# Kernel tuning notes

Measured on AMD Instinct MI355X. Metric: run time of the kernel, lower is better.

## Reference

```python
import jax, jax.numpy as jnp
import numpy as np

N = 65536       # active voxels
C = 128         # embed_channels
DEPTH = 4
NSEG = 1024     # number of clusters per level
K = 27          # 3x3x3 kernel taps
LRELU = 0.01
EPS_BN = 1e-5


def _bn(x, g, b):
    # training-mode batchnorm over the voxel axis (biased variance, as torch)
    m = jnp.mean(x, axis=0)
    v = jnp.var(x, axis=0)
    return (x - m) * jax.lax.rsqrt(v + EPS_BN) * g + b


def _lrelu(x):
    return jnp.where(x >= 0, x, LRELU * x)


def _proj(x, w, g, b):
    # Linear(bias=False) -> BatchNorm1d -> LeakyReLU
    return _lrelu(_bn(x @ w, g, b))


def setup_inputs() -> dict:
    key = jax.random.key(0)
    ks = jax.random.split(key, 24)
    s = 1.0 / np.sqrt(C)
    sc = 1.0 / np.sqrt(K * C)
    u = lambda k, shp, sk: jax.random.uniform(k, shp, jnp.float32, -sk, sk)
    g = lambda k, shp: 1.0 + 0.1 * jax.random.normal(k, shp, jnp.float32)
    inp = {}
    inp['feat'] = jax.random.normal(ks[0], (N, C), jnp.float32)
    inp['clusters'] = jax.random.randint(ks[1], (DEPTH - 1, N), 0, NSEG)
    # neighbor table for 3x3x3 sparse conv; value == N means neighbor absent
    inp['neighbor_idx'] = jax.random.randint(ks[2], (N, K), 0, N + 1)
    inp['lw_w'] = u(ks[3], (DEPTH - 1, C, C), s)
    inp['lw_gamma'] = g(ks[4], (DEPTH - 1, C))
    inp['lw_beta'] = 0.1 * jax.random.normal(ks[5], (DEPTH - 1, C), jnp.float32)
    inp['w_w'] = u(ks[6], (DEPTH - 1, C, C), s)
    inp['proj_w'] = u(ks[7], (DEPTH, C, C), s)
    inp['proj_gamma'] = g(ks[8], (DEPTH, C))
    inp['proj_beta'] = 0.1 * jax.random.normal(ks[9], (DEPTH, C), jnp.float32)
    inp['adaptive_w'] = u(ks[10], (C, DEPTH - 1), s)
    inp['fuse_w'] = u(ks[11], (2 * C, C), 1.0 / np.sqrt(2 * C))
    inp['fuse_gamma'] = g(ks[12], (C,))
    inp['fuse_beta'] = 0.1 * jax.random.normal(ks[13], (C,), jnp.float32)
    inp['conv1_w'] = u(ks[14], (K, C, C), sc)
    inp['conv2_w'] = u(ks[15], (K, C, C), sc)
    inp['bn1_gamma'] = g(ks[16], (C,))
    inp['bn1_beta'] = 0.1 * jax.random.normal(ks[17], (C,), jnp.float32)
    inp['bn2_gamma'] = g(ks[18], (C,))
    inp['bn2_beta'] = 0.1 * jax.random.normal(ks[19], (C,), jnp.float32)
    return inp


def _forward(feat, clusters, neighbor_idx, lw_w, lw_gamma, lw_beta, w_w,
             proj_w, proj_gamma, proj_beta, adaptive_w, fuse_w, fuse_gamma,
             fuse_beta, conv1_w, conv2_w, bn1_gamma, bn1_beta, bn2_gamma,
             bn2_beta):
    x_in = feat
    feats = []
    for i in range(DEPTH - 1):
        c = clusters[i]
        pw = _proj(feat, lw_w[i], lw_gamma[i], lw_beta[i])          # [N,C]
        cnt = jnp.maximum(
            jax.ops.segment_sum(jnp.ones((N,), feat.dtype), c, num_segments=NSEG), 1.0)
        seg_mean = jax.ops.segment_sum(pw, c, num_segments=NSEG) / cnt[:, None]
        pw = pw - seg_mean[c]                                        # center per cluster
        pw = pw @ w_w[i]
        pw = jnp.exp(pw - jnp.max(pw))                               # global max, as in source
        pw = pw / (jax.ops.segment_sum(pw, c, num_segments=NSEG)[c] + 1e-6)
        pf = _proj(feat, proj_w[i], proj_gamma[i], proj_beta[i]) * pw
        feats.append(jax.ops.segment_sum(pf, c, num_segments=NSEG)[c])
    adp = jax.nn.softmax(feat @ adaptive_w, axis=1)                  # [N,3]
    feats = jnp.stack(feats, axis=1)                                 # [N,3,C]
    agg = jnp.einsum('ld,ldc->lc', adp, feats)                       # [N,C]
    f_last = _proj(feat, proj_w[DEPTH - 1], proj_gamma[DEPTH - 1], proj_beta[DEPTH - 1])
    fused = _proj(jnp.concatenate([f_last, agg], axis=1), fuse_w, fuse_gamma, fuse_beta) + x_in
    residual = fused
    # 3x3x3 sparse conv on fixed topology: 27 masked gathers + per-tap GEMM
    mask = (neighbor_idx < N).astype(fused.dtype)                    # [N,K]
    idx = jnp.minimum(neighbor_idx, N - 1)

    def sconv(x, w):
        out = jnp.zeros((N, C), x.dtype)
        for k in range(K):
            out = out + (jnp.take(x, idx[:, k], axis=0) * mask[:, k:k + 1]) @ w[k]
        return out

    d = _lrelu(_bn(sconv(fused, conv1_w), bn1_gamma, bn1_beta))
    d = _lrelu(_bn(sconv(d, conv2_w), bn2_gamma, bn2_beta) + residual)
    return d


def reference(feat, clusters, neighbor_idx, lw_w, lw_gamma, lw_beta, w_w,
              proj_w, proj_gamma, proj_beta, adaptive_w, fuse_w, fuse_gamma,
              fuse_beta, conv1_w, conv2_w, bn1_gamma, bn1_beta, bn2_gamma,
              bn2_beta):
    return _forward(feat, clusters, neighbor_idx, lw_w, lw_gamma, lw_beta,
                    w_w, proj_w, proj_gamma, proj_beta, adaptive_w, fuse_w,
                    fuse_gamma, fuse_beta, conv1_w, conv2_w, bn1_gamma,
                    bn1_beta, bn2_gamma, bn2_beta)
```

## Files before the change

kernel.cpp:

```cpp
#include <hip/hip_runtime.h>

typedef unsigned short u16;
typedef unsigned int u32;
typedef __attribute__((ext_vector_type(8))) short bf16x8;
typedef __attribute__((ext_vector_type(4))) float f32x4;
typedef __attribute__((ext_vector_type(4))) u32 u32x4;

#define NROWS 65536
#define CCH 128
#define PE ((size_t)65537*128)

__device__ __forceinline__ float bf2f(u16 x){ u32 u=((u32)x)<<16; return __builtin_bit_cast(float,u); }
__device__ __forceinline__ u16 f2bf(float f){ u32 u=__builtin_bit_cast(u32,f); u += 0x7fffu + ((u>>16)&1u); return (u16)(u>>16); }
__device__ __forceinline__ float lrelu(float v){ return v>=0.f? v : 0.01f*v; }
__device__ __forceinline__ u32 fenc(float f){ u32 u=__builtin_bit_cast(u32,f); return (u & 0x80000000u) ? ~u : (u | 0x80000000u); }
__device__ __forceinline__ float fdec(u32 u){ u32 b = (u & 0x80000000u) ? (u ^ 0x80000000u) : ~u; return __builtin_bit_cast(float,b); }

__global__ __launch_bounds__(256) void prep_transpose(
    const float* __restrict__ lw, const float* __restrict__ ww, const float* __restrict__ pj,
    const float* __restrict__ fw, const float* __restrict__ c1, const float* __restrict__ c2,
    u16* __restrict__ WT)
{
  int i = blockIdx.x*256 + threadIdx.x;
  float v;
  if (i < 49152)      { int j=i;        int m=j>>14,e=j&16383,n=e>>7,k=e&127; v=lw[(m<<14)+(k<<7)+n]; }
  else if (i < 98304) { int j=i-49152;  int m=j>>14,e=j&16383,n=e>>7,k=e&127; v=ww[(m<<14)+(k<<7)+n]; }
  else if (i < 163840){ int j=i-98304;  int m=j>>14,e=j&16383,n=e>>7,k=e&127; v=pj[(m<<14)+(k<<7)+n]; }
  else if (i < 196608){ int j=i-163840; int n=j>>8, k=j&255;                  v=fw[(k<<7)+n]; }
  else if (i < 638976){ int j=i-196608; int m=j>>14,e=j&16383,n=e>>7,k=e&127; v=c1[(m<<14)+(k<<7)+n]; }
  else                { int j=i-638976; int m=j>>14,e=j&16383,n=e>>7,k=e&127; v=c2[(m<<14)+(k<<7)+n]; }
  WT[i]=f2bf(v);
}

__global__ __launch_bounds__(256) void nbrT_k(const int* __restrict__ nbr, int* __restrict__ nbrT){
  __shared__ int s[64*27];
  int b = blockIdx.x;
  for (int i=threadIdx.x; i<64*27; i+=256) s[i] = nbr[b*64*27 + i];
  __syncthreads();
  for (int i=threadIdx.x; i<64*27; i+=256){
    int tap=i>>6, row=i&63;
    nbrT[(size_t)tap*NROWS + b*64 + row] = s[row*27 + tap];
  }
}

__global__ __launch_bounds__(256) void hist_k(const int* __restrict__ cl, int* __restrict__ cnt){
  int i = blockIdx.x*256 + threadIdx.x;
  int l = i>>16;
  atomicAdd(&cnt[l*1024 + cl[i]], 1);
}
__global__ __launch_bounds__(1024) void scan_k(const int* __restrict__ cnt, int* __restrict__ starts, int* __restrict__ cur){
  int l = blockIdx.x, t = threadIdx.x;
  __shared__ int s[1024];
  int v = cnt[l*1024+t];
  s[t]=v; __syncthreads();
  for (int off=1; off<1024; off<<=1){
    int u_ = (t>=off) ? s[t-off] : 0;
    __syncthreads();
    s[t] += u_;
    __syncthreads();
  }
  int incl=s[t], excl=incl-v;
  starts[l*1025+t]=excl;
  if (t==1023) starts[l*1025+1024]=incl;
  cur[l*1024+t]=excl;
}
__global__ __launch_bounds__(256) void scatter_k(const int* __restrict__ cl, int* __restrict__ cur, int* __restrict__ order){
  int i = blockIdx.x*256 + threadIdx.x;
  int l = i>>16;
  int c = cl[i];
  int p = atomicAdd(&cur[l*1024+c], 1);
  order[l*65536 + p] = i & 65535;
}

struct BS7 { const u16* BT[7]; u16* out[7]; float* stats[7]; };

__global__ __launch_bounds__(256,2) void gemm_feat7(const float* __restrict__ feat, BS7 p)
{
  const int tid=threadIdx.x, lane=tid&63, quad=lane>>4, l15=lane&15;
  const int w=tid>>6, rh=w>>1, chq=w&1;
  const int row0=blockIdx.x*128;

  __shared__ __align__(16) u16 ldsA[128*136];
  __shared__ float cs[256];

  #pragma unroll
  for (int it=0; it<8; ++it){
    int row = it*16 + (tid>>4), chn = tid&15;
    const float* Af = feat + (size_t)(row0+row)*CCH + chn*8;
    float4 lo = *(const float4*)(Af);
    float4 hi = *(const float4*)(Af+4);
    u32x4 d;
    d[0]=(u32)f2bf(lo.x)|((u32)f2bf(lo.y)<<16);
    d[1]=(u32)f2bf(lo.z)|((u32)f2bf(lo.w)<<16);
    d[2]=(u32)f2bf(hi.x)|((u32)f2bf(hi.y)<<16);
    d[3]=(u32)f2bf(hi.z)|((u32)f2bf(hi.w)<<16);
    *(u32x4*)(&ldsA[row*136 + chn*8]) = d;
  }
  __syncthreads();

  #pragma unroll 1
  for (int y=0; y<7; ++y){
    const u16* Bb = p.BT[y];
    f32x4 acc[4][4];
    #pragma unroll
    for (int a_=0;a_<4;++a_)
      #pragma unroll
      for (int b_=0;b_<4;++b_) acc[a_][b_]=(f32x4){0.f,0.f,0.f,0.f};
    #pragma unroll
    for (int ks=0; ks<4; ++ks){
      bf16x8 af[4], bfv[4];
      #pragma unroll
      for (int mb=0;mb<4;++mb)
        af[mb]=*(const bf16x8*)(&ldsA[(rh*64+mb*16+l15)*136 + ks*32 + quad*8]);
      #pragma unroll
      for (int nb=0;nb<4;++nb)
        bfv[nb]=*(const bf16x8*)(Bb + (size_t)(chq*64+nb*16+l15)*CCH + ks*32 + quad*8);
      #pragma unroll
      for (int mb=0;mb<4;++mb)
        #pragma unroll
        for (int nb=0;nb<4;++nb)
          acc[mb][nb]=__builtin_amdgcn_mfma_f32_16x16x32_bf16(af[mb],bfv[nb],acc[mb][nb],0,0,0);
    }
    u16* O = p.out[y];
    #pragma unroll
    for (int mb=0;mb<4;++mb){
      int rbase=row0+rh*64+mb*16+quad*4;
      #pragma unroll
      for (int e=0;e<4;++e)
        #pragma unroll
        for (int nb=0;nb<4;++nb)
          O[(size_t)(rbase+e)*CCH + chq*64+nb*16+l15]=f2bf(acc[mb][nb][e]);
    }
    __syncthreads();
    cs[tid]=0.f;
    __syncthreads();
    #pragma unroll
    for (int nb=0;nb<4;++nb){
      float s=0.f,s2=0.f;
      #pragma unroll
      for (int mb=0;mb<4;++mb)
        #pragma unroll
        for (int e=0;e<4;++e){ float v=acc[mb][nb][e]; s+=v; s2+=v*v; }
      s += __shfl_xor(s,16);  s += __shfl_xor(s,32);
      s2+= __shfl_xor(s2,16); s2+= __shfl_xor(s2,32);
      if (lane<16){
        int col=chq*64+nb*16+l15;
        atomicAdd(&cs[col],s); atomicAdd(&cs[128+col],s2);
      }
    }
    __syncthreads();
    atomicAdd(&p.stats[y][tid], cs[tid]);
  }
}

struct BS3 { const u16* A[3]; const u16* BT[3]; float* out[3]; u32* gmax[3]; };

__global__ __launch_bounds__(256,2) void gemm_w3(BS3 p)
{
  const int tid=threadIdx.x, lane=tid&63, quad=lane>>4, l15=lane&15;
  const int w=tid>>6, rh=w>>1, chq=w&1;
  const int row0=blockIdx.x*128;
  const int y=blockIdx.y;

  __shared__ __align__(16) u16 ldsA[128*136];
  __shared__ float wred[4];

  const u16* A = p.A[y];
  #pragma unroll
  for (int it=0; it<8; ++it){
    int row = it*16 + (tid>>4), chn = tid&15;
    *(u32x4*)(&ldsA[row*136 + chn*8]) = *(const u32x4*)(A + (size_t)(row0+row)*CCH + chn*8);
  }
  __syncthreads();

  const u16* Bb = p.BT[y];
  f32x4 acc[4][4];
  #pragma unroll
  for (int a_=0;a_<4;++a_)
    #pragma unroll
    for (int b_=0;b_<4;++b_) acc[a_][b_]=(f32x4){0.f,0.f,0.f,0.f};
  #pragma unroll
  for (int ks=0; ks<4; ++ks){
    bf16x8 af[4], bfv[4];
    #pragma unroll
    for (int mb=0;mb<4;++mb)
      af[mb]=*(const bf16x8*)(&ldsA[(rh*64+mb*16+l15)*136 + ks*32 + quad*8]);
    #pragma unroll
    for (int nb=0;nb<4;++nb)
      bfv[nb]=*(const bf16x8*)(Bb + (size_t)(chq*64+nb*16+l15)*CCH + ks*32 + quad*8);
    #pragma unroll
    for (int mb=0;mb<4;++mb)
      #pragma unroll
      for (int nb=0;nb<4;++nb)
        acc[mb][nb]=__builtin_amdgcn_mfma_f32_16x16x32_bf16(af[mb],bfv[nb],acc[mb][nb],0,0,0);
  }
  float* O = p.out[y];
  float m=-3.0e38f;
  #pragma unroll
  for (int mb=0;mb<4;++mb){
    int rbase=row0+rh*64+mb*16+quad*4;
    #pragma unroll
    for (int e=0;e<4;++e)
      #pragma unroll
      for (int nb=0;nb<4;++nb){
        float v=acc[mb][nb][e];
        O[(size_t)(rbase+e)*CCH + chq*64+nb*16+l15]=v;
        m=fmaxf(m,v);
      }
  }
  #pragma unroll
  for (int o=1;o<64;o<<=1) m=fmaxf(m,__shfl_xor(m,o));
  if (lane==0) wred[w]=m;
  __syncthreads();
  if (tid==0){
    float mm=fmaxf(fmaxf(wred[0],wred[1]),fmaxf(wred[2],wred[3]));
    atomicMax(p.gmax[y], fenc(mm));
  }
}

__global__ __launch_bounds__(256,2) void gemm_fuse(
    const u16* __restrict__ A0, const u16* __restrict__ A1,
    const float* __restrict__ tstat, const float* __restrict__ tg, const float* __restrict__ tb,
    const u16* __restrict__ BT, u16* __restrict__ out, float* __restrict__ stats)
{
  const int tid=threadIdx.x, lane=tid&63, quad=lane>>4, l15=lane&15;
  const int w=tid>>6, rh=w>>1, chq=w&1;
  const int row0=blockIdx.x*128;

  __shared__ __align__(16) u16 ldsA[128*136];
  __shared__ float tsc[128], tsh[128];
  __shared__ float cs[256];

  if (tid<128){
    float s=tstat[tid], s2=tstat[128+tid];
    float mean=s*(1.0f/65536.0f);
    float var =s2*(1.0f/65536.0f)-mean*mean;
    float rstd=rsqrtf(var+1e-5f);
    float scv =tg[tid]*rstd;
    tsc[tid]=scv; tsh[tid]=tb[tid]-mean*scv;
  }

  f32x4 acc[4][4];
  #pragma unroll
  for (int a_=0;a_<4;++a_)
    #pragma unroll
    for (int b_=0;b_<4;++b_) acc[a_][b_]=(f32x4){0.f,0.f,0.f,0.f};

  #pragma unroll 1
  for (int tap=0; tap<2; ++tap){
    __syncthreads();
    const u16* Ab = tap ? A1 : A0;
    #pragma unroll
    for (int it=0; it<8; ++it){
      int row = it*16 + (tid>>4), chn = tid&15;
      u32x4 d = *(const u32x4*)(Ab + (size_t)(row0+row)*CCH + chn*8);
      if (tap==0){
        #pragma unroll
        for (int pq=0;pq<4;++pq){
          u32 xv=d[pq]; int k=chn*8+2*pq;
          float f0=lrelu(tsc[k  ]*bf2f((u16)(xv&0xffffu))+tsh[k  ]);
          float f1=lrelu(tsc[k+1]*bf2f((u16)(xv>>16))    +tsh[k+1]);
          d[pq]=(u32)f2bf(f0)|((u32)f2bf(f1)<<16);
        }
      }
      *(u32x4*)(&ldsA[row*136 + chn*8]) = d;
    }
    __syncthreads();
    const u16* Bb = BT + tap*128;
    #pragma unroll
    for (int ks=0; ks<4; ++ks){
      bf16x8 af[4], bfv[4];
      #pragma unroll
      for (int mb=0;mb<4;++mb)
        af[mb]=*(const bf16x8*)(&ldsA[(rh*64+mb*16+l15)*136 + ks*32 + quad*8]);
      #pragma unroll
      for (int nb=0;nb<4;++nb)
        bfv[nb]=*(const bf16x8*)(Bb + (size_t)(chq*64+nb*16+l15)*256 + ks*32 + quad*8);
      #pragma unroll
      for (int mb=0;mb<4;++mb)
        #pragma unroll
        for (int nb=0;nb<4;++nb)
          acc[mb][nb]=__builtin_amdgcn_mfma_f32_16x16x32_bf16(af[mb],bfv[nb],acc[mb][nb],0,0,0);
    }
  }
  #pragma unroll
  for (int mb=0;mb<4;++mb){
    int rbase=row0+rh*64+mb*16+quad*4;
    #pragma unroll
    for (int e=0;e<4;++e)
      #pragma unroll
      for (int nb=0;nb<4;++nb)
        out[(size_t)(rbase+e)*CCH + chq*64+nb*16+l15]=f2bf(acc[mb][nb][e]);
  }
  __syncthreads();
  cs[tid]=0.f;
  __syncthreads();
  #pragma unroll
  for (int nb=0;nb<4;++nb){
    float s=0.f,s2=0.f;
    #pragma unroll
    for (int mb=0;mb<4;++mb)
      #pragma unroll
      for (int e=0;e<4;++e){ float v=acc[mb][nb][e]; s+=v; s2+=v*v; }
    s += __shfl_xor(s,16);  s += __shfl_xor(s,32);
    s2+= __shfl_xor(s2,16); s2+= __shfl_xor(s2,32);
    if (lane<16){
      int col=chq*64+nb*16+l15;
      atomicAdd(&cs[col],s); atomicAdd(&cs[128+col],s2);
    }
  }
  __syncthreads();
  atomicAdd(&stats[tid], cs[tid]);
}

__global__ __launch_bounds__(256,2) void conv_k(
    const u16* __restrict__ A, const u16* __restrict__ BT,
    const int* __restrict__ nbrT, u16* __restrict__ out, float* __restrict__ stats)
{
  const int tid=threadIdx.x, lane=tid&63, quad=lane>>4, l15=lane&15;
  const int w=tid>>6, rh=w>>1, chq=w&1;
  const int row0=blockIdx.x*128;
  const int srow=tid>>4, schn=tid&15;

  __shared__ __align__(16) u16 bufA[2][128*136];
  __shared__ float cs[256];

  u32x4 pre[8];
  int idxn[8];
  #pragma unroll
  for (int it=0; it<8; ++it){
    int arow = nbrT[row0 + it*16 + srow];
    pre[it] = *(const u32x4*)(A + (size_t)arow*CCH + schn*8);
  }
  #pragma unroll
  for (int it=0; it<8; ++it)
    idxn[it] = nbrT[(size_t)NROWS + row0 + it*16 + srow];
  #pragma unroll
  for (int it=0; it<8; ++it)
    *(u32x4*)(&bufA[0][(it*16+srow)*136 + schn*8]) = pre[it];
  __syncthreads();

  f32x4 acc[4][4];
  #pragma unroll
  for (int a_=0;a_<4;++a_)
    #pragma unroll
    for (int b_=0;b_<4;++b_) acc[a_][b_]=(f32x4){0.f,0.f,0.f,0.f};

  #pragma unroll 1
  for (int tap=0; tap<27; ++tap){
    const int cur = tap&1, nxt = cur^1;
    if (tap<26){
      #pragma unroll
      for (int it=0; it<8; ++it)
        pre[it] = *(const u32x4*)(A + (size_t)idxn[it]*CCH + schn*8);
      if (tap<25){
        #pragma unroll
        for (int it=0; it<8; ++it)
          idxn[it] = nbrT[(size_t)(tap+2)*NROWS + row0 + it*16 + srow];
      }
    }
    const u16* Bb = BT + tap*16384;
    #pragma unroll
    for (int ks=0; ks<4; ++ks){
      bf16x8 af[4], bfv[4];
      #pragma unroll
      for (int mb=0;mb<4;++mb)
        af[mb]=*(const bf16x8*)(&bufA[cur][(rh*64+mb*16+l15)*136 + ks*32 + quad*8]);
      #pragma unroll
      for (int nb=0;nb<4;++nb)
        bfv[nb]=*(const bf16x8*)(Bb + (size_t)(chq*64+nb*16+l15)*CCH + ks*32 + quad*8);
      #pragma unroll
      for (int mb=0;mb<4;++mb)
        #pragma unroll
        for (int nb=0;nb<4;++nb)
          acc[mb][nb]=__builtin_amdgcn_mfma_f32_16x16x32_bf16(af[mb],bfv[nb],acc[mb][nb],0,0,0);
    }
    if (tap<26){
      #pragma unroll
      for (int it=0; it<8; ++it)
        *(u32x4*)(&bufA[nxt][(it*16+srow)*136 + schn*8]) = pre[it];
    }
    __syncthreads();
  }

  #pragma unroll
  for (int mb=0;mb<4;++mb){
    int rbase=row0+rh*64+mb*16+quad*4;
    #pragma unroll
    for (int e=0;e<4;++e)
      #pragma unroll
      for (int nb=0;nb<4;++nb)
        out[(size_t)(rbase+e)*CCH + chq*64+nb*16+l15]=f2bf(acc[mb][nb][e]);
  }
  cs[tid]=0.f;
  __syncthreads();
  #pragma unroll
  for (int nb=0;nb<4;++nb){
    float s=0.f,s2=0.f;
    #pragma unroll
    for (int mb=0;mb<4;++mb)
      #pragma unroll
      for (int e=0;e<4;++e){ float v=acc[mb][nb][e]; s+=v; s2+=v*v; }
    s += __shfl_xor(s,16);  s += __shfl_xor(s,32);
    s2+= __shfl_xor(s2,16); s2+= __shfl_xor(s2,32);
    if (lane<16){
      int col=chq*64+nb*16+l15;
      atomicAdd(&cs[col],s); atomicAdd(&cs[128+col],s2);
    }
  }
  __syncthreads();
  atomicAdd(&stats[tid], cs[tid]);
}

__global__ __launch_bounds__(256) void seg_bn_center_all(
    u16* __restrict__ pbase, const float* __restrict__ stats,
    const float* __restrict__ gamma, const float* __restrict__ beta,
    const int* __restrict__ starts, const int* __restrict__ order)
{
  __shared__ float sc[128], sh[128], ssum[128], smean[128];
  const int tid=threadIdx.x, b=blockIdx.x;
  const int level=b>>10, seg=b&1023;
  u16* praw = pbase + (size_t)level*PE;
  const float* st = stats + level*256;
  if (tid<128){
    float s=st[tid], s2=st[128+tid];
    float mean=s*(1.0f/65536.0f);
    float var =s2*(1.0f/65536.0f)-mean*mean;
    float rstd=rsqrtf(var+1e-5f);
    float scv =gamma[level*128+tid]*rstd;
    sc[tid]=scv; sh[tid]=beta[level*128+tid]-mean*scv;
    ssum[tid]=0.f;
  }
  __syncthreads();
  const int s0=starts[level*1025+seg], en=starts[level*1025+seg+1];
  const int c2=tid&63, half=tid>>6;
  const int* ord = order + level*65536;
  const float sc0=sc[2*c2], sc1=sc[2*c2+1], sh0=sh[2*c2], sh1=sh[2*c2+1];
  float a0=0.f, a1=0.f;
  for (int m=s0+half; m<en; m+=4){
    int r=ord[m];
    u32 x=*(const u32*)(praw + (size_t)r*CCH + 2*c2);
    a0 += lrelu(sc0*bf2f((u16)(x&0xffffu))+sh0);
    a1 += lrelu(sc1*bf2f((u16)(x>>16))    +sh1);
  }
  atomicAdd(&ssum[2*c2],a0); atomicAdd(&ssum[2*c2+1],a1);
  __syncthreads();
  if (tid<128) smean[tid]=ssum[tid]/fmaxf((float)(en-s0),1.0f);
  __syncthreads();
  const float m0=smean[2*c2], m1=smean[2*c2+1];
  for (int m=s0+half; m<en; m+=4){
    int r=ord[m];
    u32 x=*(const u32*)(praw + (size_t)r*CCH + 2*c2);
    float v0=lrelu(sc0*bf2f((u16)(x&0xffffu))+sh0)-m0;
    float v1=lrelu(sc1*bf2f((u16)(x>>16))    +sh1)-m1;
    *(u32*)(praw + (size_t)r*CCH + 2*c2) = (u32)f2bf(v0)|((u32)f2bf(v1)<<16);
  }
}

struct F3 { const float* f[3]; };
__global__ __launch_bounds__(256) void seg_softmax_all(
    F3 pw2s, const u16* __restrict__ pfbase,
    const float* __restrict__ stats, const float* __restrict__ gamma, const float* __restrict__ beta,
    const u32* __restrict__ gmax,
    const int* __restrict__ starts, const int* __restrict__ order,
    float* __restrict__ segpf)
{
  __shared__ float sc[128], sh[128], se[128], spf[128];
  const int tid=threadIdx.x, b=blockIdx.x;
  const int level=b>>10, seg=b&1023;
  const float* pw2 = pw2s.f[level];
  const u16* pfraw = pfbase + (size_t)level*PE;
  const float* st = stats + level*256;
  if (tid<128){
    float s=st[tid], s2=st[128+tid];
    float mean=s*(1.0f/65536.0f);
    float var =s2*(1.0f/65536.0f)-mean*mean;
    float rstd=rsqrtf(var+1e-5f);
    float scv =gamma[level*128+tid]*rstd;
    sc[tid]=scv; sh[tid]=beta[level*128+tid]-mean*scv;
    se[tid]=0.f; spf[tid]=0.f;
  }
  __syncthreads();
  const float M = fdec(gmax[level]);
  const int s0=starts[level*1025+seg], en=starts[level*1025+seg+1];
  const int c2=tid&63, half=tid>>6;
  const int* ord = order + level*65536;
  float a0=0.f, a1=0.f;
  for (int m=s0+half; m<en; m+=4){
    int r=ord[m];
    float2 x=*(const float2*)(pw2 + (size_t)r*CCH + 2*c2);
    a0 += __expf(x.x-M); a1 += __expf(x.y-M);
  }
  atomicAdd(&se[2*c2],a0); atomicAdd(&se[2*c2+1],a1);
  __syncthreads();
  const float d0=1.0f/(se[2*c2]+1e-6f), d1=1.0f/(se[2*c2+1]+1e-6f);
  const float sc0=sc[2*c2], sc1=sc[2*c2+1], sh0=sh[2*c2], sh1=sh[2*c2+1];
  float p0=0.f, p1=0.f;
  for (int m=s0+half; m<en; m+=4){
    int r=ord[m];
    float2 x=*(const float2*)(pw2 + (size_t)r*CCH + 2*c2);
    u32 f=*(const u32*)(pfraw + (size_t)r*CCH + 2*c2);
    p0 += lrelu(sc0*bf2f((u16)(f&0xffffu))+sh0) * (__expf(x.x-M)*d0);
    p1 += lrelu(sc1*bf2f((u16)(f>>16))    +sh1) * (__expf(x.y-M)*d1);
  }
  atomicAdd(&spf[2*c2],p0); atomicAdd(&spf[2*c2+1],p1);
  __syncthreads();
  if (tid<128) segpf[(size_t)b*128+tid]=spf[tid];
}

__global__ __launch_bounds__(256) void adp_agg(
    const float* __restrict__ feat, const float* __restrict__ aw,
    const int* __restrict__ clusters, const float* __restrict__ segpf,
    u16* __restrict__ agg)
{
  const int tid=threadIdx.x, w=tid>>6, lane=tid&63;
  const int r = blockIdx.x*4 + w;
  float t0=0.f,t1=0.f,t2=0.f;
  #pragma unroll
  for (int cc=0; cc<2; ++cc){
    int c = lane + cc*64;
    float f=feat[(size_t)r*CCH+c];
    t0 += f*aw[c*3+0];
    t1 += f*aw[c*3+1];
    t2 += f*aw[c*3+2];
  }
  #pragma unroll
  for (int o=1;o<64;o<<=1){
    t0+=__shfl_xor(t0,o); t1+=__shfl_xor(t1,o); t2+=__shfl_xor(t2,o);
  }
  float m=fmaxf(t0,fmaxf(t1,t2));
  float e0=__expf(t0-m), e1=__expf(t1-m), e2=__expf(t2-m);
  float inv=1.0f/(e0+e1+e2);
  float p0=e0*inv,p1=e1*inv,p2=e2*inv;
  int c0=clusters[r], c1_=clusters[NROWS+r], c2_=clusters[2*NROWS+r];
  const float* s0p=segpf + (size_t)c0*128;
  const float* s1p=segpf + (size_t)(1024+c1_)*128;
  const float* s2p=segpf + (size_t)(2048+c2_)*128;
  #pragma unroll
  for (int cc=0; cc<2; ++cc){
    int c = lane + cc*64;
    float v = p0*s0p[c] + p1*s1p[c] + p2*s2p[c];
    agg[(size_t)r*CCH+c]=f2bf(v);
  }
}

__global__ __launch_bounds__(256) void apply_kernel(
    const u16* __restrict__ raw, const float* __restrict__ stats,
    const float* __restrict__ g_, const float* __restrict__ b_,
    const void* __restrict__ resid, int rf32,
    void* __restrict__ out, int of32,
    int nrows, int mode)
{
  __shared__ float sc[128], sh[128];
  const int tid=threadIdx.x;
  if (tid<128){
    float s=stats[tid], s2=stats[128+tid];
    float mean=s*(1.0f/65536.0f);
    float var =s2*(1.0f/65536.0f)-mean*mean;
    float rstd=rsqrtf(var+1e-5f);
    float scv =g_[tid]*rstd;
    sc[tid]=scv; sh[tid]=b_[tid]-mean*scv;
  }
  __syncthreads();
  size_t chunk = (size_t)blockIdx.x*256 + tid;
  size_t total = (size_t)nrows*16;
  if (chunk >= total) return;
  size_t r = chunk>>4; int c8 = (int)(chunk&15)*8;
  float v[8];
  if (r >= NROWS){
    #pragma unroll
    for (int p=0;p<8;++p) v[p]=0.f;
  } else {
    u32x4 x = *(const u32x4*)(raw + r*CCH + c8);
    float rsd[8];
    if (resid){
      if (rf32){
        const float* R = ((const float*)resid) + r*CCH + c8;
        float4 lo=*(const float4*)R, hi=*(const float4*)(R+4);
        rsd[0]=lo.x; rsd[1]=lo.y; rsd[2]=lo.z; rsd[3]=lo.w;
        rsd[4]=hi.x; rsd[5]=hi.y; rsd[6]=hi.z; rsd[7]=hi.w;
      } else {
        u32x4 rv = *(const u32x4*)(((const u16*)resid) + r*CCH + c8);
        #pragma unroll
        for (int p=0;p<4;++p){
          rsd[2*p]  =bf2f((u16)(rv[p]&0xffffu));
          rsd[2*p+1]=bf2f((u16)(rv[p]>>16));
        }
      }
    } else {
      #pragma unroll
      for (int p=0;p<8;++p) rsd[p]=0.f;
    }
    #pragma unroll
    for (int p=0;p<4;++p){
      u32 xv=x[p];
      int k=c8+2*p;
      float v0=sc[k  ]*bf2f((u16)(xv&0xffffu))+sh[k  ];
      float v1=sc[k+1]*bf2f((u16)(xv>>16))    +sh[k+1];
      if (mode==0){ v[2*p]=lrelu(v0)+rsd[2*p]; v[2*p+1]=lrelu(v1)+rsd[2*p+1]; }
      else        { v[2*p]=lrelu(v0+rsd[2*p]); v[2*p+1]=lrelu(v1+rsd[2*p+1]); }
    }
  }
  if (of32){
    float* O = ((float*)out) + r*CCH + c8;
    float4 lo={v[0],v[1],v[2],v[3]}, hi={v[4],v[5],v[6],v[7]};
    *(float4*)O = lo; *(float4*)(O+4) = hi;
  } else {
    u32x4 o;
    #pragma unroll
    for (int p=0;p<4;++p) o[p] = (u32)f2bf(v[2*p]) | ((u32)f2bf(v[2*p+1])<<16);
    *(u32x4*)(((u16*)out) + r*CCH + c8) = o;
  }
}

extern "C" void kernel_launch(void* const* d_in, const int* in_sizes, int n_in,
                              void* d_out, int out_size, void* d_ws, size_t ws_size,
                              hipStream_t stream)
{
  (void)in_sizes; (void)n_in; (void)out_size; (void)ws_size;
  const float* feat = (const float*)d_in[0];
  const int* clusters = (const int*)d_in[1];
  const int* nbr  = (const int*)d_in[2];
  const float* lw_w = (const float*)d_in[3];
  const float* lw_g = (const float*)d_in[4];
  const float* lw_b = (const float*)d_in[5];
  const float* w_w  = (const float*)d_in[6];
  const float* pj_w = (const float*)d_in[7];
  const float* pj_g = (const float*)d_in[8];
  const float* pj_b = (const float*)d_in[9];
  const float* aw   = (const float*)d_in[10];
  const float* fu_w = (const float*)d_in[11];
  const float* fu_g = (const float*)d_in[12];
  const float* fu_b = (const float*)d_in[13];
  const float* c1w  = (const float*)d_in[14];
  const float* c2w  = (const float*)d_in[15];
  const float* b1g  = (const float*)d_in[16];
  const float* b1b  = (const float*)d_in[17];
  const float* b2g  = (const float*)d_in[18];
  const float* b2b  = (const float*)d_in[19];

  char* wsb = (char*)d_ws;
  u16* WT = (u16*)wsb;
  const size_t o_zero = 2162688;
  float* stats = (float*)(wsb + o_zero);
  u32*  gmax   = (u32*) (wsb + o_zero + 10240);
  int*  cnt    = (int*) (wsb + o_zero + 10496);
  int*  cur    = (int*) (wsb + o_zero + 22784);
  float* segpf = (float*)(wsb + o_zero + 35072);
  const size_t zero_bytes = 35072 + (size_t)3*1024*128*4;
  const size_t o_starts = o_zero + 1607936;
  int* starts = (int*)(wsb + o_starts);
  const size_t o_order = o_starts + 12544;
  int* order  = (int*)(wsb + o_order);
  const size_t o_pool = o_order + 786432;
  const size_t PE_B = PE*2;
  u16* A0=(u16*)(wsb+o_pool + 0*PE_B);
  u16* A1=(u16*)(wsb+o_pool + 1*PE_B);
  u16* A2=(u16*)(wsb+o_pool + 2*PE_B);
  u16* A3=(u16*)(wsb+o_pool + 3*PE_B);
  u16* A4=(u16*)(wsb+o_pool + 4*PE_B);
  u16* A5=(u16*)(wsb+o_pool + 5*PE_B);
  u16* A6=(u16*)(wsb+o_pool + 6*PE_B);
  const size_t o_F = o_pool + 7*PE_B;
  float* F0=(float*)(wsb+o_F);
  float* F1=(float*)(wsb+o_F+33554432);
  float* F2=(float*)d_out;
  int* nbrT = (int*)(wsb+o_F);

  hipMemsetAsync(wsb+o_zero, 0, zero_bytes, stream);
  prep_transpose<<<4224,256,0,stream>>>(lw_w,w_w,pj_w,fu_w,c1w,c2w,WT);
  hist_k   <<<768,256,0,stream>>>(clusters, cnt);
  scan_k   <<<3,1024,0,stream>>>(cnt, starts, cur);
  scatter_k<<<768,256,0,stream>>>(clusters, cur, order);

  const u16* lwT = WT;
  const u16* wwT = WT + 49152;
  const u16* pjT = WT + 98304;
  const u16* fuT = WT + 163840;
  const u16* c1T = WT + 196608;
  const u16* c2T = WT + 638976;

  float* stLW=stats;
  float* stPJ=stats+768;
  float* stFU=stats+1792; float* stB1=stats+2048; float* stB2=stats+2304;

  {
    BS7 p;
    for (int i=0;i<3;++i){ p.BT[i]=lwT+i*16384;     p.out[i]=A0+(size_t)i*PE; p.stats[i]=stLW+i*256; }
    for (int i=0;i<4;++i){ p.BT[3+i]=pjT+i*16384;   p.out[3+i]=(i<3)?(A3+(size_t)i*PE):A6; p.stats[3+i]=stPJ+i*256; }
    gemm_feat7<<<512,256,0,stream>>>(feat, p);
  }
  seg_bn_center_all<<<3072,256,0,stream>>>(A0, stLW, lw_g, lw_b, starts, order);
  {
    BS3 p;
    float* Fo[3]={F0,F1,F2};
    for (int i=0;i<3;++i){ p.A[i]=A0+(size_t)i*PE; p.BT[i]=wwT+i*16384; p.out[i]=Fo[i]; p.gmax[i]=gmax+i; }
    gemm_w3<<<dim3(512,3),256,0,stream>>>(p);
  }
  {
    F3 f; f.f[0]=F0; f.f[1]=F1; f.f[2]=F2;
    seg_softmax_all<<<3072,256,0,stream>>>(f, A3, stPJ, pj_g, pj_b, gmax, starts, order, segpf);
  }
  nbrT_k<<<1024,256,0,stream>>>(nbr, nbrT);
  adp_agg<<<16384,256,0,stream>>>(feat, aw, clusters, segpf, A4);
  gemm_fuse<<<512,256,0,stream>>>(A6, A4, stPJ+768, pj_g+384, pj_b+384, fuT, A5, stFU);
  apply_kernel<<<4097,256,0,stream>>>(A5, stFU, fu_g, fu_b, feat, 1, A0, 0, NROWS+1, 0);
  conv_k<<<512,256,0,stream>>>(A0, c1T, nbrT, A1, stB1);
  apply_kernel<<<4097,256,0,stream>>>(A1, stB1, b1g, b1b, nullptr, 0, A2, 0, NROWS+1, 0);
  conv_k<<<512,256,0,stream>>>(A2, c2T, nbrT, A3, stB2);
  apply_kernel<<<4096,256,0,stream>>>(A3, stB2, b2g, b2b, A0, 0, (float*)d_out, 1, NROWS, 1);
}
```

Before: 724.5 us.

## Subtract projected segment means after GEMM and fuse BN1 into second conv

The segment-centering pass is replaced by per-segment mean sums. A small GEMM projects those means through the weight, and the logits GEMM subtracts the projected segment mean by linearity, so the second read-modify-write pass over the projection tensor goes away. The logits GEMM now applies the BN and LeakyReLU on load. The separate BN1 apply kernel is fused into the second conv's gather, which also zeroes absent neighbours. The conv pipeline is restructured to prefetch two taps ahead. This adds per-element transform work inside the conv gather and changes rounding order, since the mean is subtracted after the bf16 GEMM.

```diff
diff --git a/kernel.cpp b/kernel.cpp
--- a/kernel.cpp
+++ b/kernel.cpp
@@ -153,9 +153,98 @@
   }
 }
 
-struct BS3 { const u16* A[3]; const u16* BT[3]; float* out[3]; u32* gmax[3]; };
-
-__global__ __launch_bounds__(256,2) void gemm_w3(BS3 p)
+__global__ __launch_bounds__(256) void seg_sum_all(
+    const u16* __restrict__ pbase, const float* __restrict__ stats,
+    const float* __restrict__ gamma, const float* __restrict__ beta,
+    const int* __restrict__ starts, const int* __restrict__ order,
+    u16* __restrict__ segmean)
+{
+  __shared__ float sc[128], sh[128], ssum[128];
+  const int tid=threadIdx.x, b=blockIdx.x;
+  const int level=b>>10, seg=b&1023;
+  const u16* praw = pbase + (size_t)level*PE;
+  const float* st = stats + level*256;
+  if (tid<128){
+    float s=st[tid], s2=st[128+tid];
+    float mean=s*(1.0f/65536.0f);
+    float var =s2*(1.0f/65536.0f)-mean*mean;
+    float rstd=rsqrtf(var+1e-5f);
+    float scv =gamma[level*128+tid]*rstd;
+    sc[tid]=scv; sh[tid]=beta[level*128+tid]-mean*scv;
+    ssum[tid]=0.f;
+  }
+  __syncthreads();
+  const int s0=starts[level*1025+seg], en=starts[level*1025+seg+1];
+  const int c2=tid&63, half=tid>>6;
+  const int* ord = order + level*65536;
+  const float sc0=sc[2*c2], sc1=sc[2*c2+1], sh0=sh[2*c2], sh1=sh[2*c2+1];
+  float a0=0.f, a1=0.f;
+  for (int m=s0+half; m<en; m+=4){
+    int r=ord[m];
+    u32 x=*(const u32*)(praw + (size_t)r*CCH + 2*c2);
+    a0 += lrelu(sc0*bf2f((u16)(x&0xffffu))+sh0);
+    a1 += lrelu(sc1*bf2f((u16)(x>>16))    +sh1);
+  }
+  atomicAdd(&ssum[2*c2],a0); atomicAdd(&ssum[2*c2+1],a1);
+  __syncthreads();
+  if (tid<128){
+    float inv = 1.0f/fmaxf((float)(en-s0),1.0f);
+    segmean[(size_t)b*128+tid]=f2bf(ssum[tid]*inv);
+  }
+}
+
+__global__ __launch_bounds__(256,2) void gemm_mean(
+    const u16* __restrict__ segmean, const u16* __restrict__ wwT, u16* __restrict__ segW)
+{
+  const int tid=threadIdx.x, lane=tid&63, quad=lane>>4, l15=lane&15;
+  const int w=tid>>6, rh=w>>1, chq=w&1;
+  const int row0=blockIdx.x*128;
+  const int level=row0>>10;
+  __shared__ __align__(16) u16 ldsA[128*136];
+  #pragma unroll
+  for (int it=0; it<8; ++it){
+    int row = it*16 + (tid>>4), chn = tid&15;
+    *(u32x4*)(&ldsA[row*136 + chn*8]) = *(const u32x4*)(segmean + (size_t)(row0+row)*CCH + chn*8);
+  }
+  __syncthreads();
+  const u16* Bb = wwT + level*16384;
+  f32x4 acc[4][4];
+  #pragma unroll
+  for (int a_=0;a_<4;++a_)
+    #pragma unroll
+    for (int b_=0;b_<4;++b_) acc[a_][b_]=(f32x4){0.f,0.f,0.f,0.f};
+  #pragma unroll
+  for (int ks=0; ks<4; ++ks){
+    bf16x8 af[4], bfv[4];
+    #pragma unroll
+    for (int mb=0;mb<4;++mb)
+      af[mb]=*(const bf16x8*)(&ldsA[(rh*64+mb*16+l15)*136 + ks*32 + quad*8]);
+    #pragma unroll
+    for (int nb=0;nb<4;++nb)
+      bfv[nb]=*(const bf16x8*)(Bb + (size_t)(chq*64+nb*16+l15)*CCH + ks*32 + quad*8);
+    #pragma unroll
+    for (int mb=0;mb<4;++mb)
+      #pragma unroll
+      for (int nb=0;nb<4;++nb)
+        acc[mb][nb]=__builtin_amdgcn_mfma_f32_16x16x32_bf16(af[mb],bfv[nb],acc[mb][nb],0,0,0);
+  }
+  #pragma unroll
+  for (int mb=0;mb<4;++mb){
+    int rbase=row0+rh*64+mb*16+quad*4;
+    #pragma unroll
+    for (int e=0;e<4;++e)
+      #pragma unroll
+      for (int nb=0;nb<4;++nb)
+        segW[(size_t)(rbase+e)*CCH + chq*64+nb*16+l15]=f2bf(acc[mb][nb][e]);
+  }
+}
+
+struct LG { const u16* A[3]; float* out[3]; };
+__global__ __launch_bounds__(256,2) void gemm_logits(
+    LG p, const u16* __restrict__ wwT,
+    const float* __restrict__ stats, const float* __restrict__ lwg, const float* __restrict__ lwb,
+    const int* __restrict__ clusters, const u16* __restrict__ segW,
+    u32* __restrict__ gmax)
 {
   const int tid=threadIdx.x, lane=tid&63, quad=lane>>4, l15=lane&15;
   const int w=tid>>6, rh=w>>1, chq=w&1;
@@ -163,17 +252,37 @@
   const int y=blockIdx.y;
 
   __shared__ __align__(16) u16 ldsA[128*136];
+  __shared__ float tsc[128], tsh[128];
   __shared__ float wred[4];
 
-  const u16* A = p.A[y];
+  if (tid<128){
+    const float* st = stats + y*256;
+    float s=st[tid], s2=st[128+tid];
+    float mean=s*(1.0f/65536.0f);
+    float var =s2*(1.0f/65536.0f)-mean*mean;
+    float rstd=rsqrtf(var+1e-5f);
+    float scv =lwg[y*128+tid]*rstd;
+    tsc[tid]=scv; tsh[tid]=lwb[y*128+tid]-mean*scv;
+  }
+  __syncthreads();
+
+  const u16* Ab = p.A[y];
   #pragma unroll
   for (int it=0; it<8; ++it){
     int row = it*16 + (tid>>4), chn = tid&15;
-    *(u32x4*)(&ldsA[row*136 + chn*8]) = *(const u32x4*)(A + (size_t)(row0+row)*CCH + chn*8);
-  }
-  __syncthreads();
-
-  const u16* Bb = p.BT[y];
+    u32x4 d = *(const u32x4*)(Ab + (size_t)(row0+row)*CCH + chn*8);
+    #pragma unroll
+    for (int pq=0;pq<4;++pq){
+      u32 xv=d[pq]; int k=chn*8+2*pq;
+      float f0=lrelu(tsc[k  ]*bf2f((u16)(xv&0xffffu))+tsh[k  ]);
+      float f1=lrelu(tsc[k+1]*bf2f((u16)(xv>>16))    +tsh[k+1]);
+      d[pq]=(u32)f2bf(f0)|((u32)f2bf(f1)<<16);
+    }
+    *(u32x4*)(&ldsA[row*136 + chn*8]) = d;
+  }
+  __syncthreads();
+
+  const u16* Bb = wwT + y*16384;
   f32x4 acc[4][4];
   #pragma unroll
   for (int a_=0;a_<4;++a_)
@@ -200,13 +309,18 @@
   for (int mb=0;mb<4;++mb){
     int rbase=row0+rh*64+mb*16+quad*4;
     #pragma unroll
-    for (int e=0;e<4;++e)
+    for (int e=0;e<4;++e){
+      int row=rbase+e;
+      int cl=clusters[(size_t)y*NROWS + row];
+      const u16* sw = segW + ((size_t)(y*1024+cl))*CCH;
       #pragma unroll
       for (int nb=0;nb<4;++nb){
-        float v=acc[mb][nb][e];
-        O[(size_t)(rbase+e)*CCH + chq*64+nb*16+l15]=v;
+        int col=chq*64+nb*16+l15;
+        float v=acc[mb][nb][e]-bf2f(sw[col]);
+        O[(size_t)row*CCH + col]=v;
         m=fmaxf(m,v);
       }
+    }
   }
   #pragma unroll
   for (int o=1;o<64;o<<=1) m=fmaxf(m,__shfl_xor(m,o));
@@ -214,7 +328,7 @@
   __syncthreads();
   if (tid==0){
     float mm=fmaxf(fmaxf(wred[0],wred[1]),fmaxf(wred[2],wred[3]));
-    atomicMax(p.gmax[y], fenc(mm));
+    atomicMax(&gmax[y], fenc(mm));
   }
 }
 
@@ -313,9 +427,70 @@
   atomicAdd(&stats[tid], cs[tid]);
 }
 
+template<bool TRANSA>
+__device__ __forceinline__ u32x4 conv_xf(u32x4 d, int ar, int schn,
+                                         const float* tsc, const float* tsh)
+{
+  if (TRANSA){
+    if (ar >= NROWS) return (u32x4){0u,0u,0u,0u};
+    #pragma unroll
+    for (int p=0;p<4;++p){
+      u32 xv=d[p]; int k=schn*8+2*p;
+      float f0=lrelu(tsc[k  ]*bf2f((u16)(xv&0xffffu))+tsh[k  ]);
+      float f1=lrelu(tsc[k+1]*bf2f((u16)(xv>>16))    +tsh[k+1]);
+      d[p]=(u32)f2bf(f0)|((u32)f2bf(f1)<<16);
+    }
+  }
+  return d;
+}
+
+template<bool TRANSA>
+__device__ __forceinline__ void conv_tap(
+    int tap, int cur,
+    const u16* __restrict__ A, const u16* __restrict__ BT, const int* __restrict__ nbrT,
+    int row0, int srow, int schn, int rh, int chq, int quad, int l15,
+    u16 (&bufA)[2][128*136],
+    u32x4 (&preC)[8], int (&ixC)[8], u32x4 (&preN)[8], int (&ixN)[8],
+    f32x4 (&acc)[4][4], const float* tsc, const float* tsh)
+{
+  if (tap < 25){
+    #pragma unroll
+    for (int it=0; it<8; ++it){
+      int ar = nbrT[(size_t)(tap+2)*NROWS + row0 + it*16 + srow];
+      ixN[it]=ar;
+      preN[it] = *(const u32x4*)(A + (size_t)ar*CCH + schn*8);
+    }
+  }
+  const u16* Bb = BT + tap*16384;
+  #pragma unroll
+  for (int ks=0; ks<4; ++ks){
+    bf16x8 af[4], bfv[4];
+    #pragma unroll
+    for (int mb=0;mb<4;++mb)
+      af[mb]=*(const bf16x8*)(&bufA[cur][(rh*64+mb*16+l15)*136 + ks*32 + quad*8]);
+    #pragma unroll
+    for (int nb=0;nb<4;++nb)
+      bfv[nb]=*(const bf16x8*)(Bb + (size_t)(chq*64+nb*16+l15)*CCH + ks*32 + quad*8);
+    #pragma unroll
+    for (int mb=0;mb<4;++mb)
+      #pragma unroll
+      for (int nb=0;nb<4;++nb)
+        acc[mb][nb]=__builtin_amdgcn_mfma_f32_16x16x32_bf16(af[mb],bfv[nb],acc[mb][nb],0,0,0);
+  }
+  if (tap < 26){
+    const int nxt = cur^1;
+    #pragma unroll
+    for (int it=0; it<8; ++it)
+      *(u32x4*)(&bufA[nxt][(it*16+srow)*136 + schn*8]) = conv_xf<TRANSA>(preC[it], ixC[it], schn, tsc, tsh);
+  }
+  __syncthreads();
+}
+
+template<bool TRANSA>
 __global__ __launch_bounds__(256,2) void conv_k(
     const u16* __restrict__ A, const u16* __restrict__ BT,
-    const int* __restrict__ nbrT, u16* __restrict__ out, float* __restrict__ stats)
+    const int* __restrict__ nbrT, u16* __restrict__ out, float* __restrict__ stats,
+    const float* __restrict__ tstat, const float* __restrict__ tg, const float* __restrict__ tb)
 {
   const int tid=threadIdx.x, lane=tid&63, quad=lane>>4, l15=lane&15;
   const int w=tid>>6, rh=w>>1, chq=w&1;
@@ -324,20 +499,39 @@
 
   __shared__ __align__(16) u16 bufA[2][128*136];
   __shared__ float cs[256];
-
-  u32x4 pre[8];
-  int idxn[8];
-  #pragma unroll
-  for (int it=0; it<8; ++it){
-    int arow = nbrT[row0 + it*16 + srow];
-    pre[it] = *(const u32x4*)(A + (size_t)arow*CCH + schn*8);
-  }
-  #pragma unroll
-  for (int it=0; it<8; ++it)
-    idxn[it] = nbrT[(size_t)NROWS + row0 + it*16 + srow];
-  #pragma unroll
-  for (int it=0; it<8; ++it)
-    *(u32x4*)(&bufA[0][(it*16+srow)*136 + schn*8]) = pre[it];
+  __shared__ float tsc[128], tsh[128];
+
+  if (TRANSA){
+    if (tid<128){
+      float s=tstat[tid], s2=tstat[128+tid];
+      float mean=s*(1.0f/65536.0f);
+      float var =s2*(1.0f/65536.0f)-mean*mean;
+      float rstd=rsqrtf(var+1e-5f);
+      float scv =tg[tid]*rstd;
+      tsc[tid]=scv; tsh[tid]=tb[tid]-mean*scv;
+    }
+    __syncthreads();
+  }
+
+  u32x4 pre0[8], pre1[8];
+  int   ix0[8],  ix1[8];
+
+  {
+    u32x4 t0[8]; int i0[8];
+    #pragma unroll
+    for (int it=0; it<8; ++it){
+      i0[it] = nbrT[row0 + it*16 + srow];
+      t0[it] = *(const u32x4*)(A + (size_t)i0[it]*CCH + schn*8);
+    }
+    #pragma unroll
+    for (int it=0; it<8; ++it){
+      ix0[it] = nbrT[(size_t)NROWS + row0 + it*16 + srow];
+      pre0[it] = *(const u32x4*)(A + (size_t)ix0[it]*CCH + schn*8);
+    }
+    #pragma unroll
+    for (int it=0; it<8; ++it)
+      *(u32x4*)(&bufA[0][(it*16+srow)*136 + schn*8]) = conv_xf<TRANSA>(t0[it], i0[it], schn, tsc, tsh);
+  }
   __syncthreads();
 
   f32x4 acc[4][4];
@@ -347,41 +541,11 @@
     for (int b_=0;b_<4;++b_) acc[a_][b_]=(f32x4){0.f,0.f,0.f,0.f};
 
   #pragma unroll 1
-  for (int tap=0; tap<27; ++tap){
-    const int cur = tap&1, nxt = cur^1;
-    if (tap<26){
-      #pragma unroll
-      for (int it=0; it<8; ++it)
-        pre[it] = *(const u32x4*)(A + (size_t)idxn[it]*CCH + schn*8);
-      if (tap<25){
-        #pragma unroll
-        for (int it=0; it<8; ++it)
-          idxn[it] = nbrT[(size_t)(tap+2)*NROWS + row0 + it*16 + srow];
-      }
-    }
-    const u16* Bb = BT + tap*16384;
-    #pragma unroll
-    for (int ks=0; ks<4; ++ks){
-      bf16x8 af[4], bfv[4];
-      #pragma unroll
-      for (int mb=0;mb<4;++mb)
-        af[mb]=*(const bf16x8*)(&bufA[cur][(rh*64+mb*16+l15)*136 + ks*32 + quad*8]);
-      #pragma unroll
-      for (int nb=0;nb<4;++nb)
-        bfv[nb]=*(const bf16x8*)(Bb + (size_t)(chq*64+nb*16+l15)*CCH + ks*32 + quad*8);
-      #pragma unroll
-      for (int mb=0;mb<4;++mb)
-        #pragma unroll
-        for (int nb=0;nb<4;++nb)
-          acc[mb][nb]=__builtin_amdgcn_mfma_f32_16x16x32_bf16(af[mb],bfv[nb],acc[mb][nb],0,0,0);
-    }
-    if (tap<26){
-      #pragma unroll
-      for (int it=0; it<8; ++it)
-        *(u32x4*)(&bufA[nxt][(it*16+srow)*136 + schn*8]) = pre[it];
-    }
-    __syncthreads();
-  }
+  for (int t2=0; t2<13; ++t2){
+    conv_tap<TRANSA>(2*t2,   0, A,BT,nbrT,row0,srow,schn,rh,chq,quad,l15,bufA,pre0,ix0,pre1,ix1,acc,tsc,tsh);
+    conv_tap<TRANSA>(2*t2+1, 1, A,BT,nbrT,row0,srow,schn,rh,chq,quad,l15,bufA,pre1,ix1,pre0,ix0,acc,tsc,tsh);
+  }
+  conv_tap<TRANSA>(26, 0, A,BT,nbrT,row0,srow,schn,rh,chq,quad,l15,bufA,pre0,ix0,pre1,ix1,acc,tsc,tsh);
 
   #pragma unroll
   for (int mb=0;mb<4;++mb){
@@ -410,51 +574,6 @@
   }
   __syncthreads();
   atomicAdd(&stats[tid], cs[tid]);
-}
-
-__global__ __launch_bounds__(256) void seg_bn_center_all(
-    u16* __restrict__ pbase, const float* __restrict__ stats,
-    const float* __restrict__ gamma, const float* __restrict__ beta,
-    const int* __restrict__ starts, const int* __restrict__ order)
-{
-  __shared__ float sc[128], sh[128], ssum[128], smean[128];
-  const int tid=threadIdx.x, b=blockIdx.x;
-  const int level=b>>10, seg=b&1023;
-  u16* praw = pbase + (size_t)level*PE;
-  const float* st = stats + level*256;
-  if (tid<128){
-    float s=st[tid], s2=st[128+tid];
-    float mean=s*(1.0f/65536.0f);
-    float var =s2*(1.0f/65536.0f)-mean*mean;
-    float rstd=rsqrtf(var+1e-5f);
-    float scv =gamma[level*128+tid]*rstd;
-    sc[tid]=scv; sh[tid]=beta[level*128+tid]-mean*scv;
-    ssum[tid]=0.f;
-  }
-  __syncthreads();
-  const int s0=starts[level*1025+seg], en=starts[level*1025+seg+1];
-  const int c2=tid&63, half=tid>>6;
-  const int* ord = order + level*65536;
-  const float sc0=sc[2*c2], sc1=sc[2*c2+1], sh0=sh[2*c2], sh1=sh[2*c2+1];
-  float a0=0.f, a1=0.f;
-  for (int m=s0+half; m<en; m+=4){
-    int r=ord[m];
-    u32 x=*(const u32*)(praw + (size_t)r*CCH + 2*c2);
-    a0 += lrelu(sc0*bf2f((u16)(x&0xffffu))+sh0);
-    a1 += lrelu(sc1*bf2f((u16)(x>>16))    +sh1);
-  }
-  atomicAdd(&ssum[2*c2],a0); atomicAdd(&ssum[2*c2+1],a1);
-  __syncthreads();
-  if (tid<128) smean[tid]=ssum[tid]/fmaxf((float)(en-s0),1.0f);
-  __syncthreads();
-  const float m0=smean[2*c2], m1=smean[2*c2+1];
-  for (int m=s0+half; m<en; m+=4){
-    int r=ord[m];
-    u32 x=*(const u32*)(praw + (size_t)r*CCH + 2*c2);
-    float v0=lrelu(sc0*bf2f((u16)(x&0xffffu))+sh0)-m0;
-    float v1=lrelu(sc1*bf2f((u16)(x>>16))    +sh1)-m1;
-    *(u32*)(praw + (size_t)r*CCH + 2*c2) = (u32)f2bf(v0)|((u32)f2bf(v1)<<16);
-  }
 }
 
 struct F3 { const float* f[3]; };
@@ -646,9 +765,11 @@
   u32*  gmax   = (u32*) (wsb + o_zero + 10240);
   int*  cnt    = (int*) (wsb + o_zero + 10496);
   int*  cur    = (int*) (wsb + o_zero + 22784);
+  u16*  segmean= (u16*) (wsb + o_zero + 35072);
+  u16*  segWb  = (u16*) (wsb + o_zero + 35072 + 786432);
   float* segpf = (float*)(wsb + o_zero + 35072);
-  const size_t zero_bytes = 35072 + (size_t)3*1024*128*4;
-  const size_t o_starts = o_zero + 1607936;
+  const size_t zero_bytes = 22784;
+  const size_t o_starts = o_zero + 35072 + (size_t)3*1024*128*4;
   int* starts = (int*)(wsb + o_starts);
   const size_t o_order = o_starts + 12544;
   int* order  = (int*)(wsb + o_order);
@@ -690,12 +811,13 @@
     for (int i=0;i<4;++i){ p.BT[3+i]=pjT+i*16384;   p.out[3+i]=(i<3)?(A3+(size_t)i*PE):A6; p.stats[3+i]=stPJ+i*256; }
     gemm_feat7<<<512,256,0,stream>>>(feat, p);
   }
-  seg_bn_center_all<<<3072,256,0,stream>>>(A0, stLW, lw_g, lw_b, starts, order);
+  seg_sum_all<<<3072,256,0,stream>>>(A0, stLW, lw_g, lw_b, starts, order, segmean);
+  gemm_mean<<<24,256,0,stream>>>(segmean, wwT, segWb);
   {
-    BS3 p;
+    LG p;
     float* Fo[3]={F0,F1,F2};
-    for (int i=0;i<3;++i){ p.A[i]=A0+(size_t)i*PE; p.BT[i]=wwT+i*16384; p.out[i]=Fo[i]; p.gmax[i]=gmax+i; }
-    gemm_w3<<<dim3(512,3),256,0,stream>>>(p);
+    for (int i=0;i<3;++i){ p.A[i]=A0+(size_t)i*PE; p.out[i]=Fo[i]; }
+    gemm_logits<<<dim3(512,3),256,0,stream>>>(p, wwT, stLW, lw_g, lw_b, clusters, segWb, gmax);
   }
   {
     F3 f; f.f[0]=F0; f.f[1]=F1; f.f[2]=F2;
@@ -705,8 +827,7 @@
   adp_agg<<<16384,256,0,stream>>>(feat, aw, clusters, segpf, A4);
   gemm_fuse<<<512,256,0,stream>>>(A6, A4, stPJ+768, pj_g+384, pj_b+384, fuT, A5, stFU);
   apply_kernel<<<4097,256,0,stream>>>(A5, stFU, fu_g, fu_b, feat, 1, A0, 0, NROWS+1, 0);
-  conv_k<<<512,256,0,stream>>>(A0, c1T, nbrT, A1, stB1);
-  apply_kernel<<<4097,256,0,stream>>>(A1, stB1, b1g, b1b, nullptr, 0, A2, 0, NROWS+1, 0);
-  conv_k<<<512,256,0,stream>>>(A2, c2T, nbrT, A3, stB2);
+  conv_k<false><<<512,256,0,stream>>>(A0, c1T, nbrT, A1, stB1, nullptr, nullptr, nullptr);
+  conv_k<true ><<<512,256,0,stream>>>(A1, c2T, nbrT, A3, stB2, stB1, b1g, b1b);
   apply_kernel<<<4096,256,0,stream>>>(A3, stB2, b2g, b2b, A0, 0, (float*)d_out, 1, NROWS, 1);
 }
```

Result: no change. 732.7 us (+1.1%).
